# Optimization experiments

Hardware: AMD Instinct MI355X
Metric: run time of the kernel (lower is better)

Reference implementation:

```python
import jax, jax.numpy as jnp
import numpy as np

T, H, F, E, K = 1024, 1024, 2048, 8, 2  # tokens, hidden, ffn_inter, experts, top_k


def setup_inputs() -> dict:
    key = jax.random.key(0)
    ks = jax.random.split(key, 7)
    return {
        "hidden_states": jax.random.normal(ks[0], (T, H), dtype=jnp.float32),
        "token_selected_experts": jax.random.randint(ks[1], (T, K), 0, E, dtype=jnp.int32),
        "token_final_scales": jax.random.uniform(ks[2], (T, K), dtype=jnp.float32),
        "w1": jax.random.normal(ks[3], (E, 2 * F, H), dtype=jnp.float32) * 0.02,  # gated fc1: [gate; linear]
        "b1": jax.random.normal(ks[4], (E, 2 * F), dtype=jnp.float32) * 0.02,
        "w2": jax.random.normal(ks[5], (E, H, F), dtype=jnp.float32) * 0.02,
        "b2": jax.random.normal(ks[6], (E, H), dtype=jnp.float32) * 0.02,
    }


def reference(hidden_states, token_selected_experts, token_final_scales, w1, b1, w2, b2):
    # Grouped GEMM fc1 over all experts: [T, E, 2F]
    h1 = jnp.einsum('th,efh->tef', hidden_states, w1) + b1[None]
    ffn = w2.shape[2]
    gate, lin = h1[..., :ffn], h1[..., ffn:]
    act = jax.nn.silu(gate) * lin                      # swiglu gated activation, [T, E, F]
    y_all = jnp.einsum('tef,ehf->teh', act, w2) + b2[None]  # fc2, [T, E, H]
    # Gather the top-k selected experts per token and combine with final scales
    sel = token_selected_experts.astype(jnp.int32)     # [T, K]
    y_sel = jnp.take_along_axis(y_all, sel[:, :, None], axis=1)  # [T, K, H]
    out = jnp.sum(y_sel * token_final_scales[:, :, None], axis=1)  # [T, H]
    return out
```

## Files before the change

kernel.cpp:

```cpp
#include <hip/hip_runtime.h>
#include <hip/hip_bf16.h>
#include <cstdint>
#include <cstddef>

#define TDIM 1024
#define HDIM 1024
#define FDIM 2048
#define NEXP 8
#define NENT 2048

typedef __bf16 bf16_t;
typedef __bf16 bf16x4 __attribute__((ext_vector_type(4)));
typedef __bf16 bf16x8 __attribute__((ext_vector_type(8)));
typedef float  f32x4  __attribute__((ext_vector_type(4)));

#define H_ELEMS  ((size_t)TDIM*HDIM)
#define W1_ELEMS ((size_t)NEXP*2*FDIM*HDIM)
#define W2_ELEMS ((size_t)NEXP*HDIM*FDIM)

#define WB_OFFSETS 0
#define WB_ETOK    64
#define WB_ESCALE  (WB_ETOK + NENT*4)
#define WB_ACT     16512
#define WB_H       (WB_ACT + (size_t)NENT*FDIM*2)
#define WB_W2BF    (WB_H + H_ELEMS*2)
#define WB_W1BF    (WB_W2BF + W2_ELEMS*2)
#define WB_NEED    (WB_W1BF + W1_ELEMS*2)

__device__ __forceinline__ void gload16(const void* g, void* l) {
  __builtin_amdgcn_global_load_lds((const __attribute__((address_space(1))) void*)g,
                                   (__attribute__((address_space(3))) void*)l, 16, 0, 0);
}

__device__ __forceinline__ bf16x8 cvt8(const float4 a, const float4 b) {
  bf16x8 o;
  o[0]=(bf16_t)a.x; o[1]=(bf16_t)a.y; o[2]=(bf16_t)a.z; o[3]=(bf16_t)a.w;
  o[4]=(bf16_t)b.x; o[5]=(bf16_t)b.y; o[6]=(bf16_t)b.z; o[7]=(bf16_t)b.w;
  return o;
}

__device__ __forceinline__ int segswz(int seg, int row) {
  return seg ^ (row & 3) ^ ((row >> 2) & 3);
}

__global__ void route_all(const int* __restrict__ sel, const float* __restrict__ scal,
                          int* __restrict__ offsets, int* __restrict__ etok,
                          float* __restrict__ escale) {
  __shared__ int cnt[NEXP], cnt2[NEXP], offs[NEXP+1];
  const int t = threadIdx.x;
  if (t < NEXP) { cnt[t] = 0; cnt2[t] = 0; }
  __syncthreads();
  int e8[8];
  #pragma unroll
  for (int q = 0; q < 8; q++) {
    int i = t*8 + q;
    e8[q] = sel[i];
    atomicAdd(&cnt[e8[q]], 1);
  }
  __syncthreads();
  if (t == 0) {
    int s = 0;
    for (int e = 0; e < NEXP; e++) { offs[e] = s; offsets[e] = s; s += cnt[e]; }
    offs[NEXP] = s; offsets[NEXP] = s;
  }
  __syncthreads();
  #pragma unroll
  for (int q = 0; q < 8; q++) {
    int i = t*8 + q;
    int e = e8[q];
    int pos = offs[e] + atomicAdd(&cnt2[e], 1);
    etok[pos]   = i >> 1;
    escale[pos] = scal[i];
  }
}

__global__ void convert_h(const float* __restrict__ h, bf16_t* __restrict__ hbf) {
  size_t idx = ((size_t)blockIdx.x*256 + threadIdx.x) * 8;
  float4 v0 = ((const float4*)(h + idx))[0];
  float4 v1 = ((const float4*)(h + idx))[1];
  *(bf16x8*)(hbf + idx) = cvt8(v0, v1);
}


__global__ __launch_bounds__(256, 3) void gemm1_v11(
    const bf16_t* __restrict__ hbf, const bf16_t* __restrict__ w1bf,
    const float* __restrict__ b1, const int* __restrict__ offsets,
    const int* __restrict__ etok, bf16_t* __restrict__ act)
{
  const int e   = blockIdx.y;
  const int off = offsets[e];
  const int nt  = offsets[e+1] - off;
  const int m0  = blockIdx.z * 128;
  if (m0 >= nt) return;
  const int n0  = blockIdx.x * 64;

  __shared__ __align__(16) bf16_t As[3][128*32];
  __shared__ __align__(16) bf16_t Bg[3][64*32];
  __shared__ __align__(16) bf16_t Bl[3][64*32];

  const int tid  = threadIdx.x;
  const int w    = tid >> 6, lane = tid & 63;
  const int quad = lane >> 4, lr = lane & 15;
  const int wm   = w >> 1,  wn = w & 1;

  const bf16_t* asrc0; const bf16_t* asrc1;
  int arow0, arow1;
  {
    const int r0 = 0*64 + w*16 + (lane >> 2);
    const int r1 = 1*64 + w*16 + (lane >> 2);
    const int s0 = segswz(lane & 3, r0);
    const int s1 = segswz(lane & 3, r1);
    int e0 = m0 + r0; if (e0 > nt-1) e0 = nt-1;
    int e1 = m0 + r1; if (e1 > nt-1) e1 = nt-1;
    asrc0 = hbf + (size_t)etok[off + e0]*HDIM + s0*8;
    asrc1 = hbf + (size_t)etok[off + e1]*HDIM + s1*8;
    arow0 = (0*64 + w*16)*32;
    arow1 = (1*64 + w*16)*32;
  }

  const bf16_t* gsrc; const bf16_t* lsrc;
  int bdst;
  {
    const int brow = w*16 + (lane >> 2);
    const int bseg = segswz(lane & 3, brow);
    gsrc = w1bf + ((size_t)e*2*FDIM + (size_t)(n0 + brow))*HDIM + bseg*8;
    lsrc = gsrc + (size_t)FDIM*HDIM;
    bdst = (w*16)*32;
  }

  int aoff[4], boff[2];
  #pragma unroll
  for (int i = 0; i < 4; i++) {
    const int r = wm*64 + i*16 + lr;
    aoff[i] = r*32 + (segswz(quad, r) << 3);
  }
  #pragma unroll
  for (int j = 0; j < 2; j++) {
    const int r = wn*32 + j*16 + lr;
    boff[j] = r*32 + (segswz(quad, r) << 3);
  }

  f32x4 accg[4][2] = {}, accl[4][2] = {};

#define G1_STAGE(K0, NXT)                                                     \
  { gload16(asrc0 + (K0), &As[NXT][arow0]);                                   \
    gload16(asrc1 + (K0), &As[NXT][arow1]);                                   \
    gload16(gsrc  + (K0), &Bg[NXT][bdst]);                                    \
    gload16(lsrc  + (K0), &Bl[NXT][bdst]); }

#define G1_MFMA(CUR)                                                          \
  { bf16x8 af[4], gf[2], lf[2];                                               \
    _Pragma("unroll")                                                         \
    for (int i = 0; i < 4; i++) af[i] = *(const bf16x8*)&As[CUR][aoff[i]];    \
    _Pragma("unroll")                                                         \
    for (int j = 0; j < 2; j++) {                                             \
      gf[j] = *(const bf16x8*)&Bg[CUR][boff[j]];                              \
      lf[j] = *(const bf16x8*)&Bl[CUR][boff[j]];                              \
    }                                                                         \
    _Pragma("unroll")                                                         \
    for (int i = 0; i < 4; i++)                                               \
      _Pragma("unroll")                                                       \
      for (int j = 0; j < 2; j++) {                                           \
        accg[i][j] = __builtin_amdgcn_mfma_f32_16x16x32_bf16(af[i], gf[j], accg[i][j], 0, 0, 0); \
        accl[i][j] = __builtin_amdgcn_mfma_f32_16x16x32_bf16(af[i], lf[j], accl[i][j], 0, 0, 0); \
      } }

#define G1_STEP(CUR, NXT)                                                     \
  { G1_STAGE(k0 + 64, NXT);                                                   \
    __builtin_amdgcn_sched_barrier(0);                                        \
    G1_MFMA(CUR);                                                             \
    asm volatile("s_waitcnt vmcnt(4)" ::: "memory");                          \
    __builtin_amdgcn_sched_barrier(0);                                        \
    __builtin_amdgcn_s_barrier();                                             \
    __builtin_amdgcn_sched_barrier(0);                                        \
    k0 += 32; }

  G1_STAGE(0, 0);
  G1_STAGE(32, 1);
  asm volatile("s_waitcnt vmcnt(4)" ::: "memory");
  __builtin_amdgcn_sched_barrier(0);
  __builtin_amdgcn_s_barrier();
  __builtin_amdgcn_sched_barrier(0);

  int k0 = 0;
  while (k0 < 960) {
    G1_STEP(0, 2);
    G1_STEP(1, 0);
    G1_STEP(2, 1);
  }
  G1_MFMA(0);
  asm volatile("s_waitcnt vmcnt(0)" ::: "memory");
  __builtin_amdgcn_sched_barrier(0);
  __builtin_amdgcn_s_barrier();
  __builtin_amdgcn_sched_barrier(0);
  G1_MFMA(1);

#undef G1_STEP
#undef G1_MFMA
#undef G1_STAGE

  #pragma unroll
  for (int j = 0; j < 2; j++) {
    const int f = n0 + wn*32 + j*16 + lr;
    const float bg_ = b1[e*2*FDIM + f];
    const float bl_ = b1[e*2*FDIM + FDIM + f];
    #pragma unroll
    for (int i = 0; i < 4; i++) {
      #pragma unroll
      for (int r = 0; r < 4; r++) {
        const int m = wm*64 + i*16 + quad*4 + r;
        if (m0 + m < nt) {
          const float g = accg[i][j][r] + bg_;
          const float l = accl[i][j][r] + bl_;
          const float s = g / (1.f + __expf(-g)) * l;
          act[(size_t)(off + m0 + m)*FDIM + f] = (bf16_t)s;
        }
      }
    }
  }
}

__global__ __launch_bounds__(256, 3) void gemm2_v11(
    const bf16_t* __restrict__ act, const bf16_t* __restrict__ w2bf,
    const float* __restrict__ b2, const int* __restrict__ offsets,
    const int* __restrict__ etok, const float* __restrict__ escale,
    float* __restrict__ out)
{
  const int e   = blockIdx.y;
  const int off = offsets[e];
  const int nt  = offsets[e+1] - off;
  const int m0  = blockIdx.z * 128;
  if (m0 >= nt) return;
  const int n0  = (blockIdx.x >> 2) * 128;
  const int kc  = blockIdx.x & 3;
  const int kbeg = kc * (FDIM/4);

  __shared__ __align__(16) bf16_t As[3][128*32];
  __shared__ __align__(16) bf16_t Bs[3][128*32];

  const int tid  = threadIdx.x;
  const int w    = tid >> 6, lane = tid & 63;
  const int quad = lane >> 4, lr = lane & 15;
  const int wm   = w >> 1,  wn = w & 1;

  const bf16_t* asrc0; const bf16_t* asrc1;
  int arow0, arow1;
  {
    const int r0 = 0*64 + w*16 + (lane >> 2);
    const int r1 = 1*64 + w*16 + (lane >> 2);
    const int s0 = segswz(lane & 3, r0);
    const int s1 = segswz(lane & 3, r1);
    int e0 = m0 + r0; if (e0 > nt-1) e0 = nt-1;
    int e1 = m0 + r1; if (e1 > nt-1) e1 = nt-1;
    asrc0 = act + (size_t)(off + e0)*FDIM + kbeg + s0*8;
    asrc1 = act + (size_t)(off + e1)*FDIM + kbeg + s1*8;
    arow0 = (0*64 + w*16)*32;
    arow1 = (1*64 + w*16)*32;
  }

  const bf16_t* bsrc0; const bf16_t* bsrc1;
  int bdst0, bdst1;
  {
    const int r0 = w*32 + (lane >> 2);
    const int r1 = w*32 + 16 + (lane >> 2);
    const int s0 = segswz(lane & 3, r0);
    const int s1 = segswz(lane & 3, r1);
    bsrc0 = w2bf + ((size_t)e*HDIM + (size_t)(n0 + r0))*FDIM + kbeg + s0*8;
    bsrc1 = w2bf + ((size_t)e*HDIM + (size_t)(n0 + r1))*FDIM + kbeg + s1*8;
    bdst0 = (w*32)*32;
    bdst1 = (w*32 + 16)*32;
  }

  int aoff[4], boff[4];
  #pragma unroll
  for (int i = 0; i < 4; i++) {
    const int r = wm*64 + i*16 + lr;
    aoff[i] = r*32 + (segswz(quad, r) << 3);
  }
  #pragma unroll
  for (int j = 0; j < 4; j++) {
    const int r = wn*64 + j*16 + lr;
    boff[j] = r*32 + (segswz(quad, r) << 3);
  }

  f32x4 acc[4][4] = {};

#define G2_STAGE(K0, NXT)                                                     \
  { gload16(asrc0 + (K0), &As[NXT][arow0]);                                   \
    gload16(asrc1 + (K0), &As[NXT][arow1]);                                   \
    gload16(bsrc0 + (K0), &Bs[NXT][bdst0]);                                   \
    gload16(bsrc1 + (K0), &Bs[NXT][bdst1]); }

#define G2_MFMA(CUR)                                                          \
  { bf16x8 af[4], bfr[4];                                                     \
    _Pragma("unroll")                                                         \
    for (int i = 0; i < 4; i++) af[i] = *(const bf16x8*)&As[CUR][aoff[i]];    \
    _Pragma("unroll")                                                         \
    for (int j = 0; j < 4; j++) bfr[j] = *(const bf16x8*)&Bs[CUR][boff[j]];   \
    _Pragma("unroll")                                                         \
    for (int i = 0; i < 4; i++)                                               \
      _Pragma("unroll")                                                       \
      for (int j = 0; j < 4; j++)                                             \
        acc[i][j] = __builtin_amdgcn_mfma_f32_16x16x32_bf16(af[i], bfr[j], acc[i][j], 0, 0, 0); }

#define G2_STEP(CUR, NXT)                                                     \
  { G2_STAGE(k0 + 64, NXT);                                                   \
    __builtin_amdgcn_sched_barrier(0);                                        \
    G2_MFMA(CUR);                                                             \
    asm volatile("s_waitcnt vmcnt(4)" ::: "memory");                          \
    __builtin_amdgcn_sched_barrier(0);                                        \
    __builtin_amdgcn_s_barrier();                                             \
    __builtin_amdgcn_sched_barrier(0);                                        \
    k0 += 32; }

  G2_STAGE(0, 0);
  G2_STAGE(32, 1);
  asm volatile("s_waitcnt vmcnt(4)" ::: "memory");
  __builtin_amdgcn_sched_barrier(0);
  __builtin_amdgcn_s_barrier();
  __builtin_amdgcn_sched_barrier(0);

  int k0 = 0;
  while (k0 < 384) {
    G2_STEP(0, 2);
    G2_STEP(1, 0);
    G2_STEP(2, 1);
  }
  G2_STEP(0, 2);
  G2_STEP(1, 0);
  G2_MFMA(2);
  asm volatile("s_waitcnt vmcnt(0)" ::: "memory");
  __builtin_amdgcn_sched_barrier(0);
  __builtin_amdgcn_s_barrier();
  __builtin_amdgcn_sched_barrier(0);
  G2_MFMA(0);

#undef G2_STEP
#undef G2_MFMA
#undef G2_STAGE

  #pragma unroll
  for (int i = 0; i < 4; i++) {
    #pragma unroll
    for (int r = 0; r < 4; r++) {
      const int m = wm*64 + i*16 + quad*4 + r;
      if (m0 + m < nt) {
        const int slot = off + m0 + m;
        const int t    = etok[slot];
        const float s  = escale[slot];
        #pragma unroll
        for (int j = 0; j < 4; j++) {
          const int n = n0 + wn*64 + j*16 + lr;
          float v = acc[i][j][r];
          if (kc == 0) v += b2[e*HDIM + n];
          atomicAdd(&out[(size_t)t*HDIM + n], s * v);
        }
      }
    }
  }
}

__global__ __launch_bounds__(256, 3) void gemm1_v8(
    const bf16_t* __restrict__ hbf, const float* __restrict__ w1,
    const float* __restrict__ b1, const int* __restrict__ offsets,
    const int* __restrict__ etok, bf16_t* __restrict__ act)
{
  const int e   = blockIdx.y;
  const int off = offsets[e];
  const int nt  = offsets[e+1] - off;
  const int m0  = blockIdx.z * 128;
  if (m0 >= nt) return;
  const int n0  = blockIdx.x * 64;

  __shared__ __align__(16) bf16_t As[2][128*32];
  __shared__ __align__(16) bf16_t Bg[2][64*32];
  __shared__ __align__(16) bf16_t Bl[2][64*32];

  const int tid  = threadIdx.x;
  const int w    = tid >> 6, lane = tid & 63;
  const int quad = lane >> 4, lr = lane & 15;
  const int wm   = w >> 1,  wn = w & 1;

  const bf16_t* asrc0; const bf16_t* asrc1;
  int arow0, arow1;
  {
    const int r0 = 0*64 + w*16 + (lane >> 2);
    const int r1 = 1*64 + w*16 + (lane >> 2);
    const int s0 = segswz(lane & 3, r0);
    const int s1 = segswz(lane & 3, r1);
    int e0 = m0 + r0; if (e0 > nt-1) e0 = nt-1;
    int e1 = m0 + r1; if (e1 > nt-1) e1 = nt-1;
    asrc0 = hbf + (size_t)etok[off + e0]*HDIM + s0*8;
    asrc1 = hbf + (size_t)etok[off + e1]*HDIM + s1*8;
    arow0 = (0*64 + w*16)*32;
    arow1 = (1*64 + w*16)*32;
  }

  const int br = tid >> 2, bs = tid & 3;
  const float* gsrc = w1 + ((size_t)e*2*FDIM + (size_t)(n0 + br))*HDIM + bs*8;
  const float* lsrc = gsrc + (size_t)FDIM*HDIM;
  const int bofs = br*32 + (segswz(bs, br) << 3);

  int aoff[4], boff[2];
  #pragma unroll
  for (int i = 0; i < 4; i++) {
    const int r = wm*64 + i*16 + lr;
    aoff[i] = r*32 + (segswz(quad, r) << 3);
  }
  #pragma unroll
  for (int j = 0; j < 2; j++) {
    const int r = wn*32 + j*16 + lr;
    boff[j] = r*32 + (segswz(quad, r) << 3);
  }

  f32x4 accg[4][2] = {}, accl[4][2] = {};
  float4 g4[2][2], l4[2][2];

#define F1_LOADB(SET, K0)                                                     \
  { const float4* p_ = (const float4*)(gsrc + (K0));                          \
    g4[SET][0]=p_[0]; g4[SET][1]=p_[1];                                       \
    const float4* q_ = (const float4*)(lsrc + (K0));                          \
    l4[SET][0]=q_[0]; l4[SET][1]=q_[1]; }
#define F1_WRITEB(NXT, SET)                                                   \
  { *(bf16x8*)&Bg[NXT][bofs] = cvt8(g4[SET][0], g4[SET][1]);                  \
    *(bf16x8*)&Bl[NXT][bofs] = cvt8(l4[SET][0], l4[SET][1]); }
#define F1_MFMA(CUR)                                                          \
  { bf16x8 af[4], gf[2], lf[2];                                               \
    _Pragma("unroll")                                                         \
    for (int i = 0; i < 4; i++) af[i] = *(const bf16x8*)&As[CUR][aoff[i]];    \
    _Pragma("unroll")                                                         \
    for (int j = 0; j < 2; j++) {                                             \
      gf[j] = *(const bf16x8*)&Bg[CUR][boff[j]];                              \
      lf[j] = *(const bf16x8*)&Bl[CUR][boff[j]];                              \
    }                                                                         \
    _Pragma("unroll")                                                         \
    for (int i = 0; i < 4; i++)                                               \
      _Pragma("unroll")                                                       \
      for (int j = 0; j < 2; j++) {                                           \
        accg[i][j] = __builtin_amdgcn_mfma_f32_16x16x32_bf16(af[i], gf[j], accg[i][j], 0, 0, 0); \
        accl[i][j] = __builtin_amdgcn_mfma_f32_16x16x32_bf16(af[i], lf[j], accl[i][j], 0, 0, 0); \
      } }

  F1_LOADB(0, 0);
  __builtin_amdgcn_sched_barrier(0);
  gload16(asrc0 + 0, &As[0][arow0]);
  gload16(asrc1 + 0, &As[0][arow1]);
  __builtin_amdgcn_sched_barrier(0);
  F1_WRITEB(0, 0);
  F1_LOADB(0, 32);
  F1_LOADB(1, 64);
  asm volatile("s_waitcnt vmcnt(8) lgkmcnt(0)" ::: "memory");
  __builtin_amdgcn_sched_barrier(0);
  __builtin_amdgcn_s_barrier();
  __builtin_amdgcn_sched_barrier(0);

#define F1_STEP(CUR, SET)                                                     \
  { F1_WRITEB((CUR)^1, SET);                                                  \
    __builtin_amdgcn_sched_barrier(0);                                        \
    gload16(asrc0 + k0 + 32, &As[(CUR)^1][arow0]);                            \
    gload16(asrc1 + k0 + 32, &As[(CUR)^1][arow1]);                            \
    __builtin_amdgcn_sched_barrier(0);                                        \
    F1_LOADB(SET, k0 + 96);                                                   \
    __builtin_amdgcn_sched_barrier(0);                                        \
    F1_MFMA(CUR);                                                             \
    asm volatile("s_waitcnt vmcnt(4) lgkmcnt(0)" ::: "memory");               \
    __builtin_amdgcn_sched_barrier(0);                                        \
    __builtin_amdgcn_s_barrier();                                             \
    __builtin_amdgcn_sched_barrier(0);                                        \
    k0 += 32; }

  int k0 = 0;
  while (k0 < 896) { F1_STEP(0, 0); F1_STEP(1, 1); }
  F1_STEP(0, 0);
  F1_WRITEB(0, 1);
  __builtin_amdgcn_sched_barrier(0);
  gload16(asrc0 + 960, &As[0][arow0]);
  gload16(asrc1 + 960, &As[0][arow1]);
  __builtin_amdgcn_sched_barrier(0);
  F1_MFMA(1);
  asm volatile("s_waitcnt vmcnt(0) lgkmcnt(0)" ::: "memory");
  __builtin_amdgcn_sched_barrier(0);
  __builtin_amdgcn_s_barrier();
  __builtin_amdgcn_sched_barrier(0);
  F1_WRITEB(1, 0);
  __builtin_amdgcn_sched_barrier(0);
  gload16(asrc0 + 992, &As[1][arow0]);
  gload16(asrc1 + 992, &As[1][arow1]);
  __builtin_amdgcn_sched_barrier(0);
  F1_MFMA(0);
  asm volatile("s_waitcnt vmcnt(0) lgkmcnt(0)" ::: "memory");
  __builtin_amdgcn_sched_barrier(0);
  __builtin_amdgcn_s_barrier();
  __builtin_amdgcn_sched_barrier(0);
  F1_MFMA(1);

#undef F1_STEP
#undef F1_MFMA
#undef F1_WRITEB
#undef F1_LOADB

  #pragma unroll
  for (int j = 0; j < 2; j++) {
    const int f = n0 + wn*32 + j*16 + lr;
    const float bg_ = b1[e*2*FDIM + f];
    const float bl_ = b1[e*2*FDIM + FDIM + f];
    #pragma unroll
    for (int i = 0; i < 4; i++) {
      #pragma unroll
      for (int r = 0; r < 4; r++) {
        const int m = wm*64 + i*16 + quad*4 + r;
        if (m0 + m < nt) {
          const float g = accg[i][j][r] + bg_;
          const float l = accl[i][j][r] + bl_;
          const float s = g / (1.f + __expf(-g)) * l;
          act[(size_t)(off + m0 + m)*FDIM + f] = (bf16_t)s;
        }
      }
    }
  }
}

__global__ __launch_bounds__(256, 3) void gemm2_v8(
    const bf16_t* __restrict__ act, const float* __restrict__ w2,
    const float* __restrict__ b2, const int* __restrict__ offsets,
    const int* __restrict__ etok, const float* __restrict__ escale,
    float* __restrict__ out)
{
  const int e   = blockIdx.y;
  const int off = offsets[e];
  const int nt  = offsets[e+1] - off;
  const int m0  = blockIdx.z * 128;
  if (m0 >= nt) return;
  const int n0  = (blockIdx.x >> 2) * 128;
  const int kc  = blockIdx.x & 3;
  const int kbeg = kc * (FDIM/4);

  __shared__ __align__(16) bf16_t As[2][128*32];
  __shared__ __align__(16) bf16_t Bs[2][128*32];

  const int tid  = threadIdx.x;
  const int w    = tid >> 6, lane = tid & 63;
  const int quad = lane >> 4, lr = lane & 15;
  const int wm   = w >> 1,  wn = w & 1;

  const bf16_t* asrc0; const bf16_t* asrc1;
  int arow0, arow1;
  {
    const int r0 = 0*64 + w*16 + (lane >> 2);
    const int r1 = 1*64 + w*16 + (lane >> 2);
    const int s0 = segswz(lane & 3, r0);
    const int s1 = segswz(lane & 3, r1);
    int e0 = m0 + r0; if (e0 > nt-1) e0 = nt-1;
    int e1 = m0 + r1; if (e1 > nt-1) e1 = nt-1;
    asrc0 = act + (size_t)(off + e0)*FDIM + kbeg + s0*8;
    asrc1 = act + (size_t)(off + e1)*FDIM + kbeg + s1*8;
    arow0 = (0*64 + w*16)*32;
    arow1 = (1*64 + w*16)*32;
  }

  const int br = tid >> 1, bc = tid & 1;
  const float* bsrc = w2 + ((size_t)e*HDIM + (size_t)(n0 + br))*FDIM + kbeg + bc*16;
  const int bofs0 = br*32 + (segswz(2*bc,   br) << 3);
  const int bofs1 = br*32 + (segswz(2*bc+1, br) << 3);

  int aoff[4], boff[4];
  #pragma unroll
  for (int i = 0; i < 4; i++) {
    const int r = wm*64 + i*16 + lr;
    aoff[i] = r*32 + (segswz(quad, r) << 3);
  }
  #pragma unroll
  for (int j = 0; j < 4; j++) {
    const int r = wn*64 + j*16 + lr;
    boff[j] = r*32 + (segswz(quad, r) << 3);
  }

  f32x4 acc[4][4] = {};
  float4 b4[2][4];

#define F2_LOADB(SET, K0)                                                     \
  { const float4* p_ = (const float4*)(bsrc + (K0));                          \
    b4[SET][0]=p_[0]; b4[SET][1]=p_[1]; b4[SET][2]=p_[2]; b4[SET][3]=p_[3]; }
#define F2_WRITEB(NXT, SET)                                                   \
  { *(bf16x8*)&Bs[NXT][bofs0] = cvt8(b4[SET][0], b4[SET][1]);                 \
    *(bf16x8*)&Bs[NXT][bofs1] = cvt8(b4[SET][2], b4[SET][3]); }
#define F2_MFMA(CUR)                                                          \
  { bf16x8 af[4], bfr[4];                                                     \
    _Pragma("unroll")                                                         \
    for (int i = 0; i < 4; i++) af[i] = *(const bf16x8*)&As[CUR][aoff[i]];    \
    _Pragma("unroll")                                                         \
    for (int j = 0; j < 4; j++) bfr[j] = *(const bf16x8*)&Bs[CUR][boff[j]];   \
    _Pragma("unroll")                                                         \
    for (int i = 0; i < 4; i++)                                               \
      _Pragma("unroll")                                                       \
      for (int j = 0; j < 4; j++)                                             \
        acc[i][j] = __builtin_amdgcn_mfma_f32_16x16x32_bf16(af[i], bfr[j], acc[i][j], 0, 0, 0); }

  F2_LOADB(0, 0);
  __builtin_amdgcn_sched_barrier(0);
  gload16(asrc0 + 0, &As[0][arow0]);
  gload16(asrc1 + 0, &As[0][arow1]);
  __builtin_amdgcn_sched_barrier(0);
  F2_WRITEB(0, 0);
  F2_LOADB(0, 32);
  F2_LOADB(1, 64);
  asm volatile("s_waitcnt vmcnt(8) lgkmcnt(0)" ::: "memory");
  __builtin_amdgcn_sched_barrier(0);
  __builtin_amdgcn_s_barrier();
  __builtin_amdgcn_sched_barrier(0);

#define F2_STEP(CUR, SET)                                                     \
  { F2_WRITEB((CUR)^1, SET);                                                  \
    __builtin_amdgcn_sched_barrier(0);                                        \
    gload16(asrc0 + k0 + 32, &As[(CUR)^1][arow0]);                            \
    gload16(asrc1 + k0 + 32, &As[(CUR)^1][arow1]);                            \
    __builtin_amdgcn_sched_barrier(0);                                        \
    F2_LOADB(SET, k0 + 96);                                                   \
    __builtin_amdgcn_sched_barrier(0);                                        \
    F2_MFMA(CUR);                                                             \
    asm volatile("s_waitcnt vmcnt(4) lgkmcnt(0)" ::: "memory");               \
    __builtin_amdgcn_sched_barrier(0);                                        \
    __builtin_amdgcn_s_barrier();                                             \
    __builtin_amdgcn_sched_barrier(0);                                        \
    k0 += 32; }

  int k0 = 0;
  while (k0 < 384) { F2_STEP(0, 0); F2_STEP(1, 1); }
  F2_STEP(0, 0);
  F2_WRITEB(0, 1);
  __builtin_amdgcn_sched_barrier(0);
  gload16(asrc0 + 448, &As[0][arow0]);
  gload16(asrc1 + 448, &As[0][arow1]);
  __builtin_amdgcn_sched_barrier(0);
  F2_MFMA(1);
  asm volatile("s_waitcnt vmcnt(0) lgkmcnt(0)" ::: "memory");
  __builtin_amdgcn_sched_barrier(0);
  __builtin_amdgcn_s_barrier();
  __builtin_amdgcn_sched_barrier(0);
  F2_WRITEB(1, 0);
  __builtin_amdgcn_sched_barrier(0);
  gload16(asrc0 + 480, &As[1][arow0]);
  gload16(asrc1 + 480, &As[1][arow1]);
  __builtin_amdgcn_sched_barrier(0);
  F2_MFMA(0);
  asm volatile("s_waitcnt vmcnt(0) lgkmcnt(0)" ::: "memory");
  __builtin_amdgcn_sched_barrier(0);
  __builtin_amdgcn_s_barrier();
  __builtin_amdgcn_sched_barrier(0);
  F2_MFMA(1);

#undef F2_STEP
#undef F2_MFMA
#undef F2_WRITEB
#undef F2_LOADB

  #pragma unroll
  for (int i = 0; i < 4; i++) {
    #pragma unroll
    for (int r = 0; r < 4; r++) {
      const int m = wm*64 + i*16 + quad*4 + r;
      if (m0 + m < nt) {
        const int slot = off + m0 + m;
        const int t    = etok[slot];
        const float s  = escale[slot];
        #pragma unroll
        for (int j = 0; j < 4; j++) {
          const int n = n0 + wn*64 + j*16 + lr;
          float v = acc[i][j][r];
          if (kc == 0) v += b2[e*HDIM + n];
          atomicAdd(&out[(size_t)t*HDIM + n], s * v);
        }
      }
    }
  }
}

extern "C" void kernel_launch(void* const* d_in, const int* in_sizes, int n_in,
                              void* d_out, int out_size, void* d_ws, size_t ws_size,
                              hipStream_t stream) {
  const float* hidden = (const float*)d_in[0];
  const int*   sel    = (const int*)d_in[1];
  const float* scal   = (const float*)d_in[2];
  const float* w1     = (const float*)d_in[3];
  const float* b1     = (const float*)d_in[4];
  const float* w2     = (const float*)d_in[5];
  const float* b2     = (const float*)d_in[6];
  float* out = (float*)d_out;

  char* ws = (char*)d_ws;
  int*    offsets = (int*)(ws + WB_OFFSETS);
  int*    etok    = (int*)(ws + WB_ETOK);
  float*  escale  = (float*)(ws + WB_ESCALE);
  bf16_t* act     = (bf16_t*)(ws + WB_ACT);
  bf16_t* hbf     = (bf16_t*)(ws + WB_H);
  bf16_t* w2bf    = (bf16_t*)(ws + WB_W2BF);
  bf16_t* w1bf    = (bf16_t*)(ws + WB_W1BF);

  hipMemsetAsync(d_out, 0, (size_t)out_size * sizeof(float), stream);

  route_all<<<1, 256, 0, stream>>>(sel, scal, offsets, etok, escale);
  convert_h<<<(int)(H_ELEMS/8/256), 256, 0, stream>>>(hidden, hbf);

  if (ws_size >= WB_NEED) {
    convert_h<<<(int)(W2_ELEMS/8/256), 256, 0, stream>>>(w2, w2bf);
    convert_h<<<(int)(W1_ELEMS/8/256), 256, 0, stream>>>(w1, w1bf);
    gemm1_v11<<<dim3(FDIM/64, NEXP, NENT/128), 256, 0, stream>>>(hbf, w1bf, b1, offsets, etok, act);
    gemm2_v11<<<dim3((HDIM/128)*4, NEXP, NENT/128), 256, 0, stream>>>(act, w2bf, b2, offsets, etok, escale, out);
  } else {
    gemm1_v8<<<dim3(FDIM/64, NEXP, NENT/128), 256, 0, stream>>>(hbf, w1, b1, offsets, etok, act);
    gemm2_v8<<<dim3((HDIM/128)*4, NEXP, NENT/128), 256, 0, stream>>>(act, w2, b2, offsets, etok, escale, out);
  }
}
```

Baseline: 356.9 us.

## Repack bf16 weights into tile-contiguous pre-swizzled blocks for GEMM loads

Replaces the plain fp32-to-bf16 weight conversion with repack kernels that also write w1 and w2 in tile-major order, with each 32-wide K-slice of a 64- or 128-row tile stored contiguously and already segment-swizzled. The GEMM kernels then load each B tile as one contiguous 4–8 KB chunk, with lane-linear addresses, instead of strided 64-byte row segments, and need less per-thread address arithmetic. The conversion still runs every call. The repack kernels read fp32 with a strided pattern, which may slow the conversion step, and this step is a large share of the total time.

```diff
diff --git a/kernel.cpp b/kernel.cpp
--- a/kernel.cpp
+++ b/kernel.cpp
@@ -82,8 +82,33 @@
 }
 
 
-__global__ __launch_bounds__(256, 3) void gemm1_v11(
-    const bf16_t* __restrict__ hbf, const bf16_t* __restrict__ w1bf,
+__global__ void repack_w1(const float* __restrict__ w1, bf16_t* __restrict__ w1r) {
+  const int u = blockIdx.x;
+  const int t = u & 31, p = (u >> 5) & 31, e = u >> 10;
+  const int tid = threadIdx.x;
+  const int gl = tid >> 8, slot = tid & 255;
+  const int r = slot >> 2, spos = slot & 3;
+  const int s = segswz(spos, r);
+  const float* src = w1 + ((size_t)(e*2 + gl)*FDIM + p*64 + r)*HDIM + t*32 + s*8;
+  float4 v0 = ((const float4*)src)[0];
+  float4 v1 = ((const float4*)src)[1];
+  *(bf16x8*)(w1r + (size_t)u*4096 + gl*2048 + slot*8) = cvt8(v0, v1);
+}
+
+__global__ void repack_w2(const float* __restrict__ w2, bf16_t* __restrict__ w2r) {
+  const int v = blockIdx.x;
+  const int tc = v & 63, q = (v >> 6) & 7, e = v >> 9;
+  const int tid = threadIdx.x;
+  const int r = tid >> 2, spos = tid & 3;
+  const int s = segswz(spos, r);
+  const float* src = w2 + ((size_t)e*HDIM + q*128 + r)*FDIM + tc*32 + s*8;
+  float4 v0 = ((const float4*)src)[0];
+  float4 v1 = ((const float4*)src)[1];
+  *(bf16x8*)(w2r + (size_t)v*4096 + tid*8) = cvt8(v0, v1);
+}
+
+__global__ __launch_bounds__(256, 3) void gemm1_v12(
+    const bf16_t* __restrict__ hbf, const bf16_t* __restrict__ w1r,
     const float* __restrict__ b1, const int* __restrict__ offsets,
     const int* __restrict__ etok, bf16_t* __restrict__ act)
 {
@@ -92,7 +117,8 @@
   const int nt  = offsets[e+1] - off;
   const int m0  = blockIdx.z * 128;
   if (m0 >= nt) return;
-  const int n0  = blockIdx.x * 64;
+  const int p   = blockIdx.x;
+  const int n0  = p * 64;
 
   __shared__ __align__(16) bf16_t As[3][128*32];
   __shared__ __align__(16) bf16_t Bg[3][64*32];
@@ -118,15 +144,8 @@
     arow1 = (1*64 + w*16)*32;
   }
 
-  const bf16_t* gsrc; const bf16_t* lsrc;
-  int bdst;
-  {
-    const int brow = w*16 + (lane >> 2);
-    const int bseg = segswz(lane & 3, brow);
-    gsrc = w1bf + ((size_t)e*2*FDIM + (size_t)(n0 + brow))*HDIM + bseg*8;
-    lsrc = gsrc + (size_t)FDIM*HDIM;
-    bdst = (w*16)*32;
-  }
+  const bf16_t* gW1 = w1r + ((size_t)(e*32 + p)*32)*4096 + w*512 + lane*8;
+  const int bofsw = w*512;
 
   int aoff[4], boff[2];
   #pragma unroll
@@ -145,8 +164,8 @@
 #define G1_STAGE(K0, NXT)                                                     \
   { gload16(asrc0 + (K0), &As[NXT][arow0]);                                   \
     gload16(asrc1 + (K0), &As[NXT][arow1]);                                   \
-    gload16(gsrc  + (K0), &Bg[NXT][bdst]);                                    \
-    gload16(lsrc  + (K0), &Bl[NXT][bdst]); }
+    gload16(gW1 + (size_t)(K0)*128,        &Bg[NXT][bofsw]);                  \
+    gload16(gW1 + (size_t)(K0)*128 + 2048, &Bl[NXT][bofsw]); }
 
 #define G1_MFMA(CUR)                                                          \
   { bf16x8 af[4], gf[2], lf[2];                                               \
@@ -220,8 +239,8 @@
   }
 }
 
-__global__ __launch_bounds__(256, 3) void gemm2_v11(
-    const bf16_t* __restrict__ act, const bf16_t* __restrict__ w2bf,
+__global__ __launch_bounds__(256, 3) void gemm2_v12(
+    const bf16_t* __restrict__ act, const bf16_t* __restrict__ w2r,
     const float* __restrict__ b2, const int* __restrict__ offsets,
     const int* __restrict__ etok, const float* __restrict__ escale,
     float* __restrict__ out)
@@ -231,7 +250,8 @@
   const int nt  = offsets[e+1] - off;
   const int m0  = blockIdx.z * 128;
   if (m0 >= nt) return;
-  const int n0  = (blockIdx.x >> 2) * 128;
+  const int q   = blockIdx.x >> 2;
+  const int n0  = q * 128;
   const int kc  = blockIdx.x & 3;
   const int kbeg = kc * (FDIM/4);
 
@@ -258,18 +278,8 @@
     arow1 = (1*64 + w*16)*32;
   }
 
-  const bf16_t* bsrc0; const bf16_t* bsrc1;
-  int bdst0, bdst1;
-  {
-    const int r0 = w*32 + (lane >> 2);
-    const int r1 = w*32 + 16 + (lane >> 2);
-    const int s0 = segswz(lane & 3, r0);
-    const int s1 = segswz(lane & 3, r1);
-    bsrc0 = w2bf + ((size_t)e*HDIM + (size_t)(n0 + r0))*FDIM + kbeg + s0*8;
-    bsrc1 = w2bf + ((size_t)e*HDIM + (size_t)(n0 + r1))*FDIM + kbeg + s1*8;
-    bdst0 = (w*32)*32;
-    bdst1 = (w*32 + 16)*32;
-  }
+  const bf16_t* bW2 = w2r + ((size_t)((e*8 + q)*64 + kc*16))*4096 + w*1024 + lane*8;
+  const int bofsw = w*1024;
 
   int aoff[4], boff[4];
   #pragma unroll
@@ -288,8 +298,8 @@
 #define G2_STAGE(K0, NXT)                                                     \
   { gload16(asrc0 + (K0), &As[NXT][arow0]);                                   \
     gload16(asrc1 + (K0), &As[NXT][arow1]);                                   \
-    gload16(bsrc0 + (K0), &Bs[NXT][bdst0]);                                   \
-    gload16(bsrc1 + (K0), &Bs[NXT][bdst1]); }
+    gload16(bW2 + (size_t)(K0)*128,       &Bs[NXT][bofsw]);                   \
+    gload16(bW2 + (size_t)(K0)*128 + 512, &Bs[NXT][bofsw + 512]); }
 
 #define G2_MFMA(CUR)                                                          \
   { bf16x8 af[4], bfr[4];                                                     \
@@ -693,8 +703,8 @@
   float*  escale  = (float*)(ws + WB_ESCALE);
   bf16_t* act     = (bf16_t*)(ws + WB_ACT);
   bf16_t* hbf     = (bf16_t*)(ws + WB_H);
-  bf16_t* w2bf    = (bf16_t*)(ws + WB_W2BF);
-  bf16_t* w1bf    = (bf16_t*)(ws + WB_W1BF);
+  bf16_t* w2r     = (bf16_t*)(ws + WB_W2BF);
+  bf16_t* w1r     = (bf16_t*)(ws + WB_W1BF);
 
   hipMemsetAsync(d_out, 0, (size_t)out_size * sizeof(float), stream);
 
@@ -702,10 +712,10 @@
   convert_h<<<(int)(H_ELEMS/8/256), 256, 0, stream>>>(hidden, hbf);
 
   if (ws_size >= WB_NEED) {
-    convert_h<<<(int)(W2_ELEMS/8/256), 256, 0, stream>>>(w2, w2bf);
-    convert_h<<<(int)(W1_ELEMS/8/256), 256, 0, stream>>>(w1, w1bf);
-    gemm1_v11<<<dim3(FDIM/64, NEXP, NENT/128), 256, 0, stream>>>(hbf, w1bf, b1, offsets, etok, act);
-    gemm2_v11<<<dim3((HDIM/128)*4, NEXP, NENT/128), 256, 0, stream>>>(act, w2bf, b2, offsets, etok, escale, out);
+    repack_w2<<<NEXP*8*64, 512, 0, stream>>>(w2, w2r);
+    repack_w1<<<NEXP*32*32, 512, 0, stream>>>(w1, w1r);
+    gemm1_v12<<<dim3(FDIM/64, NEXP, NENT/128), 256, 0, stream>>>(hbf, w1r, b1, offsets, etok, act);
+    gemm2_v12<<<dim3((HDIM/128)*4, NEXP, NENT/128), 256, 0, stream>>>(act, w2r, b2, offsets, etok, escale, out);
   } else {
     gemm1_v8<<<dim3(FDIM/64, NEXP, NENT/128), 256, 0, stream>>>(hbf, w1, b1, offsets, etok, act);
     gemm2_v8<<<dim3((HDIM/128)*4, NEXP, NENT/128), 256, 0, stream>>>(act, w2, b2, offsets, etok, escale, out);
```

After: 365.1 us. 1.02x slower.
